# Optimization experiments

Measured on AMD Instinct MI355X. Metric: run time of the kernel, lower is better.

Reference implementation:

```python
import jax, jax.numpy as jnp
import numpy as np

B, N, NH, H = 32, 512, 4, 32      # batch, agents per group, heads, hidden per head
IN_DIM, OUT_DIM = 128, 128
BIG = 9.0e15
SQRT_DK = float(np.sqrt(H))


def setup_inputs() -> dict:
    key = jax.random.key(0)
    keys = iter(jax.random.split(key, 64))

    def nrm(shape, scale=0.05):
        return jax.random.normal(next(keys), shape, dtype=jnp.float32) * scale

    inp = {}
    inp["x0"] = jax.random.normal(next(keys), (B, N, IN_DIM), dtype=jnp.float32)
    inp["x1"] = jax.random.normal(next(keys), (B, N, IN_DIM), dtype=jnp.float32)
    for name in ("m00", "m01", "m10", "m11"):
        inp[name] = jax.random.randint(next(keys), (B, N, N), 0, 2, dtype=jnp.int32)
    # per-group q/k/v projections: Linear(in_dim, NH*H)
    for g in (0, 1):
        inp[f"wq{g}"] = nrm((IN_DIM, NH * H)); inp[f"bq{g}"] = nrm((NH * H,))
        inp[f"wk{g}"] = nrm((IN_DIM, NH * H)); inp[f"bk{g}"] = nrm((NH * H,))
        inp[f"wv{g}"] = nrm((IN_DIM, NH * H)); inp[f"bv{g}"] = nrm((NH * H,))
    # fc_outs[i][j]: Linear(NH*H, H)
    for i in (0, 1):
        for j in (0, 1):
            inp[f"wo{i}{j}"] = nrm((NH * H, H)); inp[f"bo{i}{j}"] = nrm((H,))
    # fc_out_final[i]: Linear(H * 2, out_dim)
    for g in (0, 1):
        inp[f"wf{g}"] = nrm((2 * H, OUT_DIM)); inp[f"bf{g}"] = nrm((OUT_DIM,))
    return inp


def _qkv(x, wq, bq, wk, bk, wv, bv):
    q = jax.nn.relu(x @ wq + bq)
    k = jax.nn.relu(x @ wk + bk)
    v = jax.nn.relu(x @ wv + bv)
    return q, k, v


def _split_heads(t):
    # [B, N, NH*H] -> [B, NH, N, H]; contiguous H-blocks == torch per-head slices
    return t.reshape(B, t.shape[1], NH, H).transpose(0, 2, 1, 3)


def _attend(q, k, v, mask, gate):
    qh, kh, vh = _split_heads(q), _split_heads(k), _split_heads(v)
    logits = jnp.einsum('bhqd,bhkd->bhqk', qh, kh) / SQRT_DK
    m = mask.astype(logits.dtype)[:, None]            # [B,1,Nq,Nk]
    w = jax.nn.softmax(logits * m - BIG * (1.0 - m), axis=-1)
    if gate:
        has = (mask.sum(axis=-1) > 0).astype(w.dtype)  # [B,Nq]
        w = w * has[:, None, :, None]
    out = jnp.einsum('bhqk,bhkd->bhqd', w, vh)
    # heads concatenated along feature dim (matches torch.cat of head slices)
    return out.transpose(0, 2, 1, 3).reshape(B, q.shape[1], NH * H)


def reference(x0, x1, m00, m01, m10, m11,
              wq0, bq0, wk0, bk0, wv0, bv0,
              wq1, bq1, wk1, bk1, wv1, bv1,
              wo00, bo00, wo01, bo01, wo10, bo10, wo11, bo11,
              wf0, bf0, wf1, bf1):
    q0, k0, v0 = _qkv(x0, wq0, bq0, wk0, bk0, wv0, bv0)
    q1, k1, v1 = _qkv(x1, wq1, bq1, wk1, bk1, wv1, bv1)
    inner0 = jax.nn.relu(_attend(q0, k0, v0, m00, gate=False) @ wo00 + bo00)
    inner1 = jax.nn.relu(_attend(q1, k1, v1, m11, gate=False) @ wo11 + bo11)
    inter0 = jax.nn.relu(_attend(q0, k1, v1, m01, gate=True) @ wo01 + bo01)
    inter1 = jax.nn.relu(_attend(q1, k0, v0, m10, gate=True) @ wo10 + bo10)
    out0 = jnp.concatenate([inner0, inter0], axis=-1) @ wf0 + bf0
    out1 = jnp.concatenate([inner1, inter1], axis=-1) @ wf1 + bf1
    return (out0, out1)
```

## Files before the change

kernel.cpp:

```cpp
#include <hip/hip_runtime.h>

#define B_    32
#define N_    512
#define D_    128
#define ROWS  (B_ * N_)
#define SCALE2_ (0.17677669529663687f * 1.4426950408889634f)

typedef __bf16 bf16x8 __attribute__((ext_vector_type(8)));
typedef __bf16 bf16x4 __attribute__((ext_vector_type(4)));
typedef float  f32x4  __attribute__((ext_vector_type(4)));

static __device__ __forceinline__ f32x4 mfma16(bf16x8 a, bf16x8 b, f32x4 c) {
  return __builtin_amdgcn_mfma_f32_16x16x32_bf16(a, b, c, 0, 0, 0);
}

__global__ __launch_bounds__(256) void prep_kernel(
    const int* __restrict__ m00, const int* __restrict__ m01,
    const int* __restrict__ m10, const int* __restrict__ m11,
    const float* __restrict__ wq0, const float* __restrict__ wk0, const float* __restrict__ wv0,
    const float* __restrict__ wq1, const float* __restrict__ wk1, const float* __restrict__ wv1,
    const float* __restrict__ wo00, const float* __restrict__ wo01,
    const float* __restrict__ wo10, const float* __restrict__ wo11,
    const float* __restrict__ wf0, const float* __restrict__ wf1,
    __bf16* __restrict__ wtb, __bf16* __restrict__ wob, __bf16* __restrict__ wfb,
    unsigned long long* __restrict__ mpk)
{
  const int bx = blockIdx.x, t = threadIdx.x;
  if (bx < 16384) {
    const int wid = bx * 4 + (t >> 6);
    const int lane = t & 63;
    const int row = wid & 511, b = (wid >> 9) & 31, a = wid >> 14;
    const int* msel = (a == 0) ? m00 : (a == 1) ? m11 : (a == 2) ? m01 : m10;
    const int* src = msel + ((size_t)b * N_ + row) * N_;
    unsigned long long mine = 0;
    #pragma unroll
    for (int ch = 0; ch < 8; ++ch) {
      const int v = src[ch * 64 + lane];
      const unsigned long long bits = __ballot(v != 0);
      if (lane == ch) mine = bits;
    }
    if (lane < 8)
      mpk[((size_t)(a * 32 + b) * 8 + lane) * 512 + row] = mine;
  } else if (bx < 16480) {
    const int i = bx - 16384, mat = i >> 4, sub = i & 15;
    const float* w = (mat == 0) ? wq0 : (mat == 1) ? wk0 : (mat == 2) ? wv0
                   : (mat == 3) ? wq1 : (mat == 4) ? wk1 : wv1;
    __bf16* dst = wtb + mat * 16384;
    const int fidx = sub * 256 + t;
    const float4 f = ((const float4*)w)[fidx];
    const int e = fidx * 4, k = e >> 7, n = e & 127;
    dst[(n + 0) * 128 + k] = (__bf16)f.x;
    dst[(n + 1) * 128 + k] = (__bf16)f.y;
    dst[(n + 2) * 128 + k] = (__bf16)f.z;
    dst[(n + 3) * 128 + k] = (__bf16)f.w;
  } else if (bx < 16496) {
    const int i = bx - 16480, a = i >> 2, sub = i & 3;
    const float* w = (a == 0) ? wo00 : (a == 1) ? wo11 : (a == 2) ? wo01 : wo10;
    __bf16* dst = wob + a * 4096;
    const int fidx = sub * 256 + t;
    const float4 f = ((const float4*)w)[fidx];
    const int e = fidx * 4, k = e >> 5, n = e & 31;
    dst[(n + 0) * 128 + k] = (__bf16)f.x;
    dst[(n + 1) * 128 + k] = (__bf16)f.y;
    dst[(n + 2) * 128 + k] = (__bf16)f.z;
    dst[(n + 3) * 128 + k] = (__bf16)f.w;
  } else {
    const int i = bx - 16496, g = i >> 3, sub = i & 7;
    const float* w = g ? wf1 : wf0;
    __bf16* dst = wfb + g * 8192;
    const int d0 = sub * 1024 + t * 4;
    const int n = d0 >> 6, k = d0 & 63;
    bf16x4 v;
    #pragma unroll
    for (int j = 0; j < 4; ++j) v[j] = (__bf16)w[(size_t)(k + j) * 128 + n];
    *(bf16x4*)&dst[d0] = v;
  }
}

__global__ __launch_bounds__(256) void qkv_kernel(
    const float* __restrict__ x0, const float* __restrict__ x1,
    const float* __restrict__ bq0, const float* __restrict__ bk0, const float* __restrict__ bv0,
    const float* __restrict__ bq1, const float* __restrict__ bk1, const float* __restrict__ bv1,
    const __bf16* __restrict__ wtb, __bf16* __restrict__ qkvb)
{
  __shared__ __align__(16) __bf16 vtile[128][72];
  const int bx = blockIdx.x;
  const int g = bx >> 8, tile = bx & 255, R0 = tile * 64;
  const int t = threadIdx.x, lane = t & 63, wave = t >> 6;
  const int quad = lane >> 4, ln = lane & 15;
  const float* xs = g ? x1 : x0;

  bf16x8 af[4];
  {
    const int row = R0 + wave * 16 + ln;
    #pragma unroll
    for (int ks = 0; ks < 4; ++ks) {
      const float4* xp = (const float4*)(xs + (size_t)row * D_ + ks * 32 + quad * 8);
      float4 a = xp[0], b = xp[1];
      bf16x8 v;
      v[0] = (__bf16)a.x; v[1] = (__bf16)a.y; v[2] = (__bf16)a.z; v[3] = (__bf16)a.w;
      v[4] = (__bf16)b.x; v[5] = (__bf16)b.y; v[6] = (__bf16)b.z; v[7] = (__bf16)b.w;
      af[ks] = v;
    }
  }
  const f32x4 zero4 = {0.f, 0.f, 0.f, 0.f};

  for (int m = 0; m < 3; ++m) {
    const __bf16* wt = wtb + (g * 3 + m) * 16384;
    const float* bias = (g == 0) ? ((m == 0) ? bq0 : (m == 1) ? bk0 : bv0)
                                 : ((m == 0) ? bq1 : (m == 1) ? bk1 : bv1);
    __bf16* outp = qkvb + (size_t)(g * 3 + m) * (ROWS * D_);

    f32x4 acc[8];
    #pragma unroll
    for (int nt = 0; nt < 8; ++nt) acc[nt] = zero4;
    #pragma unroll
    for (int ks = 0; ks < 4; ++ks) {
      #pragma unroll
      for (int nt = 0; nt < 8; ++nt) {
        bf16x8 bfrag = *(const bf16x8*)(wt + (size_t)(nt * 16 + ln) * D_ + ks * 32 + quad * 8);
        acc[nt] = mfma16(af[ks], bfrag, acc[nt]);
      }
    }

    if (m != 2) {
      const float sc = (m == 0) ? SCALE2_ : 1.0f;
      #pragma unroll
      for (int nt = 0; nt < 8; ++nt) {
        const int col = nt * 16 + ln;
        const float bv = bias[col];
        #pragma unroll
        for (int r = 0; r < 4; ++r) {
          float v = fmaxf(acc[nt][r] + bv, 0.f) * sc;
          outp[(size_t)(R0 + wave * 16 + quad * 4 + r) * D_ + col] = (__bf16)v;
        }
      }
    } else {
      #pragma unroll
      for (int nt = 0; nt < 8; ++nt) {
        const int col = nt * 16 + ln;
        const float bv = bias[col];
        #pragma unroll
        for (int r = 0; r < 4; ++r) {
          float v = fmaxf(acc[nt][r] + bv, 0.f);
          vtile[col][wave * 16 + quad * 4 + r] = (__bf16)v;
        }
      }
      __syncthreads();
      const int b = R0 >> 9, kb2 = R0 & 511;
      const int dim = t >> 1, off = (t & 1) * 32;
      uint4* dst = (uint4*)(outp + (size_t)b * (D_ * N_) + (size_t)dim * N_ + kb2 + off);
      const uint4* srcp = (const uint4*)&vtile[dim][off];
      #pragma unroll
      for (int i = 0; i < 4; ++i) dst[i] = srcp[i];
    }
  }
}

__global__ __launch_bounds__(256, 2) void attn_kernel(
    const __bf16* __restrict__ qkvb,
    const unsigned long long* __restrict__ mpk,
    const __bf16* __restrict__ wob,
    const float* __restrict__ bo00, const float* __restrict__ bo01,
    const float* __restrict__ bo10, const float* __restrict__ bo11,
    __bf16* __restrict__ projb)
{
  __shared__ __align__(16) __bf16 raw[18432];

  const int bx = blockIdx.x;
  const int qt = bx >> 7, cb = bx & 127, a = cb >> 5, b = cb & 31;
  const int t = threadIdx.x, lane = t & 63, h = t >> 6;
  const int quad = lane >> 4, ln = lane & 15;

  const int qg = (a == 1 || a == 3) ? 1 : 0;
  const int kg = (a == 1 || a == 2) ? 1 : 0;
  const float* bo = (a == 0) ? bo00 : (a == 1) ? bo11 : (a == 2) ? bo01 : bo10;

  const __bf16* qb  = qkvb + (size_t)(qg * 3 + 0) * (ROWS * D_) + (size_t)(b * N_ + qt * 64) * D_;
  const __bf16* kb  = qkvb + (size_t)(kg * 3 + 1) * (ROWS * D_) + (size_t)b * N_ * D_;
  const __bf16* vtb = qkvb + (size_t)(kg * 3 + 2) * (ROWS * D_) + (size_t)b * D_ * N_;
  const unsigned long long* mrow = mpk + (size_t)(a * 32 + b) * 8 * 512 + qt * 64;

  __bf16* PT = raw + h * 4608;

  bf16x8 qf[4];
  #pragma unroll
  for (int bt = 0; bt < 4; ++bt)
    qf[bt] = *(const bf16x8*)(qb + (size_t)(bt * 16 + ln) * D_ + h * 32 + quad * 8);

  const f32x4 zero4 = {0.f, 0.f, 0.f, 0.f};
  f32x4 Oacc[2][4];
  float lp[4];
  #pragma unroll
  for (int bt = 0; bt < 4; ++bt) {
    lp[bt] = 0.f;
    Oacc[0][bt] = zero4; Oacc[1][bt] = zero4;
  }

  unsigned long long mb[4];
  #pragma unroll
  for (int bt = 0; bt < 4; ++bt) mb[bt] = mrow[bt * 16 + ln];

  for (int ch = 0; ch < 8; ++ch) {
    const int kc = ch * 64;

    unsigned long long mbn[4] = {0, 0, 0, 0};
    if (ch < 7) {
      #pragma unroll
      for (int bt = 0; bt < 4; ++bt)
        mbn[bt] = mrow[(size_t)(ch + 1) * 512 + bt * 16 + ln];
    }

    #pragma unroll
    for (int at = 0; at < 4; ++at) {
      bf16x8 kf = *(const bf16x8*)(kb + (size_t)(kc + at * 16 + ln) * D_ + h * 32 + quad * 8);
      #pragma unroll
      for (int bt = 0; bt < 4; ++bt) {
        f32x4 s = mfma16(kf, qf[bt], zero4);
        bf16x4 pv;
        float ps = 0.f;
        #pragma unroll
        for (int r = 0; r < 4; ++r) {
          const int bit = (int)((mb[bt] >> (at * 16 + quad * 4 + r)) & 1ull);
          const float p = bit ? __builtin_amdgcn_exp2f(s[r]) : 0.f;
          ps += p;
          pv[r] = (__bf16)p;
        }
        lp[bt] += ps;
        *(bf16x4*)&PT[(bt * 16 + ln) * 72 + at * 16 + quad * 4] = pv;
      }
    }

    #pragma unroll
    for (int s2 = 0; s2 < 2; ++s2) {
      bf16x8 pb[4];
      #pragma unroll
      for (int bt = 0; bt < 4; ++bt)
        pb[bt] = *(const bf16x8*)&PT[(bt * 16 + ln) * 72 + s2 * 32 + quad * 8];
      #pragma unroll
      for (int d = 0; d < 2; ++d) {
        bf16x8 vf = *(const bf16x8*)(vtb + (size_t)(h * 32 + d * 16 + ln) * N_ + kc + s2 * 32 + quad * 8);
        #pragma unroll
        for (int bt = 0; bt < 4; ++bt)
          Oacc[d][bt] = mfma16(vf, pb[bt], Oacc[d][bt]);
      }
    }

    #pragma unroll
    for (int bt = 0; bt < 4; ++bt) mb[bt] = mbn[bt];
  }

  float fac[4];
  #pragma unroll
  for (int bt = 0; bt < 4; ++bt) {
    float l = lp[bt] + __shfl_xor(lp[bt], 16);
    l += __shfl_xor(l, 32);
    fac[bt] = (l > 0.f) ? 1.f / l : 0.f;
  }

  __syncthreads();
  __bf16* OL = raw;
  #pragma unroll
  for (int d = 0; d < 2; ++d)
    #pragma unroll
    for (int bt = 0; bt < 4; ++bt) {
      bf16x4 ov;
      #pragma unroll
      for (int r = 0; r < 4; ++r) ov[r] = (__bf16)(Oacc[d][bt][r] * fac[bt]);
      *(bf16x4*)&OL[(bt * 16 + ln) * 136 + h * 32 + d * 16 + quad * 4] = ov;
    }
  __syncthreads();

  const __bf16* wo = wob + a * 4096;
  f32x4 pacc[2];
  pacc[0] = zero4; pacc[1] = zero4;
  #pragma unroll
  for (int ks = 0; ks < 4; ++ks) {
    bf16x8 afr = *(const bf16x8*)&OL[(h * 16 + ln) * 136 + ks * 32 + quad * 8];
    #pragma unroll
    for (int ct = 0; ct < 2; ++ct) {
      bf16x8 bw = *(const bf16x8*)(wo + (size_t)(ct * 16 + ln) * D_ + ks * 32 + quad * 8);
      pacc[ct] = mfma16(afr, bw, pacc[ct]);
    }
  }
  const int R0g = b * N_ + qt * 64;
  #pragma unroll
  for (int ct = 0; ct < 2; ++ct) {
    const int col = ct * 16 + ln;
    const float bv = bo[col];
    #pragma unroll
    for (int r = 0; r < 4; ++r) {
      const float v = fmaxf(pacc[ct][r] + bv, 0.f);
      projb[(size_t)(a * ROWS + R0g + h * 16 + quad * 4 + r) * 32 + col] = (__bf16)v;
    }
  }
}

__global__ __launch_bounds__(256) void outproj_kernel(
    const __bf16* __restrict__ projb, const __bf16* __restrict__ wfb,
    const float* __restrict__ bf0, const float* __restrict__ bf1,
    float* __restrict__ out)
{
  const int t = threadIdx.x, lane = t & 63, w = t >> 6;
  const int quad = lane >> 4, ln = lane & 15;
  const int row = blockIdx.x * 64 + w * 16;
  const f32x4 zero4 = {0.f, 0.f, 0.f, 0.f};

  #pragma unroll
  for (int g = 0; g < 2; ++g) {
    const float* bfp = g ? bf1 : bf0;
    f32x4 acc[8];
    #pragma unroll
    for (int ct = 0; ct < 8; ++ct) acc[ct] = zero4;
    #pragma unroll
    for (int s = 0; s < 2; ++s) {
      const int asrc = s ? (2 + g) : g;
      bf16x8 afr = *(const bf16x8*)(projb + (size_t)(asrc * ROWS + row + ln) * 32 + quad * 8);
      const __bf16* wb = wfb + g * 8192 + s * 32;
      #pragma unroll
      for (int ct = 0; ct < 8; ++ct) {
        bf16x8 bw = *(const bf16x8*)(wb + (size_t)(ct * 16 + ln) * 64 + quad * 8);
        acc[ct] = mfma16(afr, bw, acc[ct]);
      }
    }
    float* og = out + (size_t)g * (ROWS * D_);
    #pragma unroll
    for (int ct = 0; ct < 8; ++ct) {
      const int col = ct * 16 + ln;
      const float bv = bfp[col];
      #pragma unroll
      for (int r = 0; r < 4; ++r)
        og[(size_t)(row + quad * 4 + r) * D_ + col] = acc[ct][r] + bv;
    }
  }
}

extern "C" void kernel_launch(void* const* d_in, const int* in_sizes, int n_in,
                              void* d_out, int out_size, void* d_ws, size_t ws_size,
                              hipStream_t stream)
{
  const float* x0 = (const float*)d_in[0];
  const float* x1 = (const float*)d_in[1];
  const int* m00 = (const int*)d_in[2];
  const int* m01 = (const int*)d_in[3];
  const int* m10 = (const int*)d_in[4];
  const int* m11 = (const int*)d_in[5];
  const float* wq0 = (const float*)d_in[6];  const float* bq0 = (const float*)d_in[7];
  const float* wk0 = (const float*)d_in[8];  const float* bk0 = (const float*)d_in[9];
  const float* wv0 = (const float*)d_in[10]; const float* bv0 = (const float*)d_in[11];
  const float* wq1 = (const float*)d_in[12]; const float* bq1 = (const float*)d_in[13];
  const float* wk1 = (const float*)d_in[14]; const float* bk1 = (const float*)d_in[15];
  const float* wv1 = (const float*)d_in[16]; const float* bv1 = (const float*)d_in[17];
  const float* wo00 = (const float*)d_in[18]; const float* bo00 = (const float*)d_in[19];
  const float* wo01 = (const float*)d_in[20]; const float* bo01 = (const float*)d_in[21];
  const float* wo10 = (const float*)d_in[22]; const float* bo10 = (const float*)d_in[23];
  const float* wo11 = (const float*)d_in[24]; const float* bo11 = (const float*)d_in[25];
  const float* wf0 = (const float*)d_in[26]; const float* bf0 = (const float*)d_in[27];
  const float* wf1 = (const float*)d_in[28]; const float* bf1 = (const float*)d_in[29];

  __bf16* qkvb = (__bf16*)d_ws;
  __bf16* projb = (__bf16*)((char*)d_ws + 25165824);
  __bf16* wtb  = (__bf16*)((char*)d_ws + 29360128);
  __bf16* wob  = (__bf16*)((char*)d_ws + 29556736);
  __bf16* wfb  = (__bf16*)((char*)d_ws + 29589504);
  unsigned long long* mpk = (unsigned long long*)((char*)d_ws + 29622272);

  prep_kernel<<<dim3(16512), dim3(256), 0, stream>>>(
      m00, m01, m10, m11, wq0, wk0, wv0, wq1, wk1, wv1,
      wo00, wo01, wo10, wo11, wf0, wf1, wtb, wob, wfb, mpk);
  qkv_kernel<<<dim3(512), dim3(256), 0, stream>>>(
      x0, x1, bq0, bk0, bv0, bq1, bk1, bv1, wtb, qkvb);
  attn_kernel<<<dim3(1024), dim3(256), 0, stream>>>(
      qkvb, mpk, wob, bo00, bo01, bo10, bo11, projb);
  outproj_kernel<<<dim3(256), dim3(256), 0, stream>>>(
      projb, wfb, bf0, bf1, (float*)d_out);
}
```

Baseline: 302.2 us.

## Keep attention probabilities in registers via permuted key rows; split QKV/outproj grids

The attention kernel permutes which key rows each lane loads, so the MFMA score output already has the layout needed as the A operand of the P·V MFMA. The probabilities therefore stay in registers instead of making a round trip through shared memory, and the per-wave P tile is dropped. The QKV kernel now launches one block per projection matrix instead of looping over Q/K/V, and the output projection launches one block per group. This gives more parallel blocks, at the cost of reloading and converting the x tile three times.

```diff
diff --git a/kernel.cpp b/kernel.cpp
--- a/kernel.cpp
+++ b/kernel.cpp
@@ -85,10 +85,15 @@
 {
   __shared__ __align__(16) __bf16 vtile[128][72];
   const int bx = blockIdx.x;
-  const int g = bx >> 8, tile = bx & 255, R0 = tile * 64;
+  const int mat = bx >> 8, tile = bx & 255, R0 = tile * 64;
+  const int m = mat % 3;
   const int t = threadIdx.x, lane = t & 63, wave = t >> 6;
   const int quad = lane >> 4, ln = lane & 15;
-  const float* xs = g ? x1 : x0;
+  const float* xs = (mat < 3) ? x0 : x1;
+  const float* bias = (mat == 0) ? bq0 : (mat == 1) ? bk0 : (mat == 2) ? bv0
+                    : (mat == 3) ? bq1 : (mat == 4) ? bk1 : bv1;
+  const __bf16* wt = wtb + mat * 16384;
+  __bf16* outp = qkvb + (size_t)mat * (ROWS * D_);
 
   bf16x8 af[4];
   {
@@ -105,55 +110,48 @@
   }
   const f32x4 zero4 = {0.f, 0.f, 0.f, 0.f};
 
-  for (int m = 0; m < 3; ++m) {
-    const __bf16* wt = wtb + (g * 3 + m) * 16384;
-    const float* bias = (g == 0) ? ((m == 0) ? bq0 : (m == 1) ? bk0 : bv0)
-                                 : ((m == 0) ? bq1 : (m == 1) ? bk1 : bv1);
-    __bf16* outp = qkvb + (size_t)(g * 3 + m) * (ROWS * D_);
-
-    f32x4 acc[8];
-    #pragma unroll
-    for (int nt = 0; nt < 8; ++nt) acc[nt] = zero4;
-    #pragma unroll
-    for (int ks = 0; ks < 4; ++ks) {
-      #pragma unroll
-      for (int nt = 0; nt < 8; ++nt) {
-        bf16x8 bfrag = *(const bf16x8*)(wt + (size_t)(nt * 16 + ln) * D_ + ks * 32 + quad * 8);
-        acc[nt] = mfma16(af[ks], bfrag, acc[nt]);
-      }
-    }
-
-    if (m != 2) {
-      const float sc = (m == 0) ? SCALE2_ : 1.0f;
-      #pragma unroll
-      for (int nt = 0; nt < 8; ++nt) {
-        const int col = nt * 16 + ln;
-        const float bv = bias[col];
-        #pragma unroll
-        for (int r = 0; r < 4; ++r) {
-          float v = fmaxf(acc[nt][r] + bv, 0.f) * sc;
-          outp[(size_t)(R0 + wave * 16 + quad * 4 + r) * D_ + col] = (__bf16)v;
-        }
-      }
-    } else {
-      #pragma unroll
-      for (int nt = 0; nt < 8; ++nt) {
-        const int col = nt * 16 + ln;
-        const float bv = bias[col];
-        #pragma unroll
-        for (int r = 0; r < 4; ++r) {
-          float v = fmaxf(acc[nt][r] + bv, 0.f);
-          vtile[col][wave * 16 + quad * 4 + r] = (__bf16)v;
-        }
-      }
-      __syncthreads();
-      const int b = R0 >> 9, kb2 = R0 & 511;
-      const int dim = t >> 1, off = (t & 1) * 32;
-      uint4* dst = (uint4*)(outp + (size_t)b * (D_ * N_) + (size_t)dim * N_ + kb2 + off);
-      const uint4* srcp = (const uint4*)&vtile[dim][off];
-      #pragma unroll
-      for (int i = 0; i < 4; ++i) dst[i] = srcp[i];
-    }
+  f32x4 acc[8];
+  #pragma unroll
+  for (int nt = 0; nt < 8; ++nt) acc[nt] = zero4;
+  #pragma unroll
+  for (int ks = 0; ks < 4; ++ks) {
+    #pragma unroll
+    for (int nt = 0; nt < 8; ++nt) {
+      bf16x8 bfrag = *(const bf16x8*)(wt + (size_t)(nt * 16 + ln) * D_ + ks * 32 + quad * 8);
+      acc[nt] = mfma16(af[ks], bfrag, acc[nt]);
+    }
+  }
+
+  if (m != 2) {
+    const float sc = (m == 0) ? SCALE2_ : 1.0f;
+    #pragma unroll
+    for (int nt = 0; nt < 8; ++nt) {
+      const int col = nt * 16 + ln;
+      const float bv = bias[col];
+      #pragma unroll
+      for (int r = 0; r < 4; ++r) {
+        float v = fmaxf(acc[nt][r] + bv, 0.f) * sc;
+        outp[(size_t)(R0 + wave * 16 + quad * 4 + r) * D_ + col] = (__bf16)v;
+      }
+    }
+  } else {
+    #pragma unroll
+    for (int nt = 0; nt < 8; ++nt) {
+      const int col = nt * 16 + ln;
+      const float bv = bias[col];
+      #pragma unroll
+      for (int r = 0; r < 4; ++r) {
+        float v = fmaxf(acc[nt][r] + bv, 0.f);
+        vtile[col][wave * 16 + quad * 4 + r] = (__bf16)v;
+      }
+    }
+    __syncthreads();
+    const int b = R0 >> 9, kb2 = R0 & 511;
+    const int dim = t >> 1, off = (t & 1) * 32;
+    uint4* dst = (uint4*)(outp + (size_t)b * (D_ * N_) + (size_t)dim * N_ + kb2 + off);
+    const uint4* srcp = (const uint4*)&vtile[dim][off];
+    #pragma unroll
+    for (int i = 0; i < 4; ++i) dst[i] = srcp[i];
   }
 }
 
@@ -165,7 +163,7 @@
     const float* __restrict__ bo10, const float* __restrict__ bo11,
     __bf16* __restrict__ projb)
 {
-  __shared__ __align__(16) __bf16 raw[18432];
+  __shared__ __align__(16) __bf16 OL[64][136];
 
   const int bx = blockIdx.x;
   const int qt = bx >> 7, cb = bx & 127, a = cb >> 5, b = cb & 31;
@@ -181,7 +179,7 @@
   const __bf16* vtb = qkvb + (size_t)(kg * 3 + 2) * (ROWS * D_) + (size_t)b * D_ * N_;
   const unsigned long long* mrow = mpk + (size_t)(a * 32 + b) * 8 * 512 + qt * 64;
 
-  __bf16* PT = raw + h * 4608;
+  const int lnoff = 8 * (ln >> 2) + (ln & 3);
 
   bf16x8 qf[4];
   #pragma unroll
@@ -211,9 +209,11 @@
         mbn[bt] = mrow[(size_t)(ch + 1) * 512 + bt * 16 + ln];
     }
 
+    bf16x4 pregs[4][4];
     #pragma unroll
     for (int at = 0; at < 4; ++at) {
-      bf16x8 kf = *(const bf16x8*)(kb + (size_t)(kc + at * 16 + ln) * D_ + h * 32 + quad * 8);
+      const int kconst = 32 * (at >> 1) + 4 * (at & 1);
+      bf16x8 kf = *(const bf16x8*)(kb + (size_t)(kc + kconst + lnoff) * D_ + h * 32 + quad * 8);
       #pragma unroll
       for (int bt = 0; bt < 4; ++bt) {
         f32x4 s = mfma16(kf, qf[bt], zero4);
@@ -221,13 +221,13 @@
         float ps = 0.f;
         #pragma unroll
         for (int r = 0; r < 4; ++r) {
-          const int bit = (int)((mb[bt] >> (at * 16 + quad * 4 + r)) & 1ull);
+          const int bit = (int)((mb[bt] >> (kconst + 8 * quad + r)) & 1ull);
           const float p = bit ? __builtin_amdgcn_exp2f(s[r]) : 0.f;
           ps += p;
           pv[r] = (__bf16)p;
         }
         lp[bt] += ps;
-        *(bf16x4*)&PT[(bt * 16 + ln) * 72 + at * 16 + quad * 4] = pv;
+        pregs[at][bt] = pv;
       }
     }
 
@@ -235,8 +235,13 @@
     for (int s2 = 0; s2 < 2; ++s2) {
       bf16x8 pb[4];
       #pragma unroll
-      for (int bt = 0; bt < 4; ++bt)
-        pb[bt] = *(const bf16x8*)&PT[(bt * 16 + ln) * 72 + s2 * 32 + quad * 8];
+      for (int bt = 0; bt < 4; ++bt) {
+        #pragma unroll
+        for (int j = 0; j < 4; ++j) {
+          pb[bt][j]     = pregs[2 * s2][bt][j];
+          pb[bt][4 + j] = pregs[2 * s2 + 1][bt][j];
+        }
+      }
       #pragma unroll
       for (int d = 0; d < 2; ++d) {
         bf16x8 vf = *(const bf16x8*)(vtb + (size_t)(h * 32 + d * 16 + ln) * N_ + kc + s2 * 32 + quad * 8);
@@ -258,8 +263,6 @@
     fac[bt] = (l > 0.f) ? 1.f / l : 0.f;
   }
 
-  __syncthreads();
-  __bf16* OL = raw;
   #pragma unroll
   for (int d = 0; d < 2; ++d)
     #pragma unroll
@@ -267,7 +270,7 @@
       bf16x4 ov;
       #pragma unroll
       for (int r = 0; r < 4; ++r) ov[r] = (__bf16)(Oacc[d][bt][r] * fac[bt]);
-      *(bf16x4*)&OL[(bt * 16 + ln) * 136 + h * 32 + d * 16 + quad * 4] = ov;
+      *(bf16x4*)&OL[bt * 16 + ln][h * 32 + d * 16 + quad * 4] = ov;
     }
   __syncthreads();
 
@@ -276,7 +279,7 @@
   pacc[0] = zero4; pacc[1] = zero4;
   #pragma unroll
   for (int ks = 0; ks < 4; ++ks) {
-    bf16x8 afr = *(const bf16x8*)&OL[(h * 16 + ln) * 136 + ks * 32 + quad * 8];
+    bf16x8 afr = *(const bf16x8*)&OL[h * 16 + ln][ks * 32 + quad * 8];
     #pragma unroll
     for (int ct = 0; ct < 2; ++ct) {
       bf16x8 bw = *(const bf16x8*)(wo + (size_t)(ct * 16 + ln) * D_ + ks * 32 + quad * 8);
@@ -301,37 +304,36 @@
     const float* __restrict__ bf0, const float* __restrict__ bf1,
     float* __restrict__ out)
 {
+  const int bx = blockIdx.x;
+  const int g = bx >> 8, tile = bx & 255;
   const int t = threadIdx.x, lane = t & 63, w = t >> 6;
   const int quad = lane >> 4, ln = lane & 15;
-  const int row = blockIdx.x * 64 + w * 16;
+  const int row = tile * 64 + w * 16;
   const f32x4 zero4 = {0.f, 0.f, 0.f, 0.f};
 
-  #pragma unroll
-  for (int g = 0; g < 2; ++g) {
-    const float* bfp = g ? bf1 : bf0;
-    f32x4 acc[8];
-    #pragma unroll
-    for (int ct = 0; ct < 8; ++ct) acc[ct] = zero4;
-    #pragma unroll
-    for (int s = 0; s < 2; ++s) {
-      const int asrc = s ? (2 + g) : g;
-      bf16x8 afr = *(const bf16x8*)(projb + (size_t)(asrc * ROWS + row + ln) * 32 + quad * 8);
-      const __bf16* wb = wfb + g * 8192 + s * 32;
-      #pragma unroll
-      for (int ct = 0; ct < 8; ++ct) {
-        bf16x8 bw = *(const bf16x8*)(wb + (size_t)(ct * 16 + ln) * 64 + quad * 8);
-        acc[ct] = mfma16(afr, bw, acc[ct]);
-      }
-    }
-    float* og = out + (size_t)g * (ROWS * D_);
+  const float* bfp = g ? bf1 : bf0;
+  f32x4 acc[8];
+  #pragma unroll
+  for (int ct = 0; ct < 8; ++ct) acc[ct] = zero4;
+  #pragma unroll
+  for (int s = 0; s < 2; ++s) {
+    const int asrc = s ? (2 + g) : g;
+    bf16x8 afr = *(const bf16x8*)(projb + (size_t)(asrc * ROWS + row + ln) * 32 + quad * 8);
+    const __bf16* wb = wfb + g * 8192 + s * 32;
     #pragma unroll
     for (int ct = 0; ct < 8; ++ct) {
-      const int col = ct * 16 + ln;
-      const float bv = bfp[col];
-      #pragma unroll
-      for (int r = 0; r < 4; ++r)
-        og[(size_t)(row + quad * 4 + r) * D_ + col] = acc[ct][r] + bv;
-    }
+      bf16x8 bw = *(const bf16x8*)(wb + (size_t)(ct * 16 + ln) * 64 + quad * 8);
+      acc[ct] = mfma16(afr, bw, acc[ct]);
+    }
+  }
+  float* og = out + (size_t)g * (ROWS * D_);
+  #pragma unroll
+  for (int ct = 0; ct < 8; ++ct) {
+    const int col = ct * 16 + ln;
+    const float bv = bfp[col];
+    #pragma unroll
+    for (int r = 0; r < 4; ++r)
+      og[(size_t)(row + quad * 4 + r) * D_ + col] = acc[ct][r] + bv;
   }
 }
 
@@ -368,10 +370,10 @@
   prep_kernel<<<dim3(16512), dim3(256), 0, stream>>>(
       m00, m01, m10, m11, wq0, wk0, wv0, wq1, wk1, wv1,
       wo00, wo01, wo10, wo11, wf0, wf1, wtb, wob, wfb, mpk);
-  qkv_kernel<<<dim3(512), dim3(256), 0, stream>>>(
+  qkv_kernel<<<dim3(1536), dim3(256), 0, stream>>>(
       x0, x1, bq0, bk0, bv0, bq1, bk1, bv1, wtb, qkvb);
   attn_kernel<<<dim3(1024), dim3(256), 0, stream>>>(
       qkvb, mpk, wob, bo00, bo01, bo10, bo11, projb);
-  outproj_kernel<<<dim3(256), dim3(256), 0, stream>>>(
+  outproj_kernel<<<dim3(512), dim3(256), 0, stream>>>(
       projb, wfb, bf0, bf1, (float*)d_out);
 }
```

Measured after the change: 301.5 us (median of 2 runs). Within noise of the previous version (-0.2%).
